# Performance work log

Measured on AMD Instinct MI355X. Metric: run time of the kernel, lower is better.

The kernel has to match this reference:

```python
import jax, jax.numpy as jnp
import numpy as np
import math

# dims
H = 2048        # hidden_size
NH = 16         # mamba_num_heads
HPH = 128       # hidden_size_per_head
I = NH * HPH    # intermediate_size = 2048
N = 64          # mamba_d_state
K = 4           # mamba_d_conv
R = max(64, H // 16)  # time_step_rank = 128
L = 2048        # total tokens (single prefill sequence)
EPS = 1e-6


def rmsnorm(x, w, eps=EPS):
    return x * jax.lax.rsqrt(jnp.mean(x * x, axis=-1, keepdims=True) + eps) * w


def setup_inputs() -> dict:
    key = jax.random.key(0)
    ks = jax.random.split(key, 12)
    s = 0.02
    # dt_bias per get_initial_dt_bias
    dt_min, dt_max = 0.001, 0.1
    u = jax.random.uniform(ks[0], (NH,))
    dt = jnp.exp(u * (math.log(dt_max) - math.log(dt_min)) + math.log(dt_min))
    dt = jnp.clip(dt, 0.0001)
    dt_bias = dt + jnp.log(-jnp.expm1(-dt))
    return {
        "hidden_states": jax.random.normal(ks[1], (L, H), jnp.float32),
        "in_proj_w": jax.random.normal(ks[2], (H, 2 * I), jnp.float32) * s,
        "conv_w": jax.random.normal(ks[3], (I, K), jnp.float32) * s,
        "bcdt_w": jax.random.normal(ks[4], (I, 2 * N + R), jnp.float32) * s,
        "dt_norm_w": jnp.ones((R,), jnp.float32),
        "B_norm_w": jnp.ones((N,), jnp.float32),
        "C_norm_w": jnp.ones((N,), jnp.float32),
        "dt_proj_w": jax.random.normal(ks[5], (R, NH), jnp.float32) * s,
        "dt_bias": dt_bias.astype(jnp.float32),
        "A": -jnp.exp(jax.random.normal(ks[6], (I, N), jnp.float32) * 0.5),  # A = -exp(A_log)
        "D": jnp.ones((I,), jnp.float32),
        "out_proj_w": jax.random.normal(ks[7], (I, H), jnp.float32) * s,
    }


def reference(hidden_states, in_proj_w, conv_w, bcdt_w, dt_norm_w, B_norm_w,
              C_norm_w, dt_proj_w, dt_bias, A, D, out_proj_w):
    # in_proj -> [L, NH, 2*HPH]; split into gate and hidden (per-head halves)
    proj = (hidden_states @ in_proj_w).reshape(L, NH, 2 * HPH)
    gate = proj[:, :, :HPH].reshape(L, I)
    hs = proj[:, :, HPH:].reshape(L, I)

    # causal depthwise conv1d along time + SiLU
    xp = jnp.pad(hs, ((K - 1, 0), (0, 0)))  # left-pad time (zero initial conv state)
    conv = sum(conv_w[:, k] * xp[k:k + L] for k in range(K))  # [L, I]
    hs = jax.nn.silu(conv)

    # B, C, dt projections + RMSNorms
    ssm_p = hs @ bcdt_w  # [L, 2N+R]
    B = rmsnorm(ssm_p[:, :N], B_norm_w)          # [L, N]
    C = rmsnorm(ssm_p[:, N:2 * N], C_norm_w)     # [L, N]
    ts = rmsnorm(ssm_p[:, 2 * N:], dt_norm_w)    # [L, R]
    dt = ts @ dt_proj_w                           # [L, NH]

    # expand per-head dt / bias to full intermediate dim, softplus discretization
    dt_full = jnp.repeat(dt, HPH, axis=1)         # [L, I]
    bias_full = jnp.repeat(dt_bias, HPH)          # [I]
    delta = jax.nn.softplus(dt_full + bias_full)  # [L, I]

    # selective scan: state [I, N], zero initial state
    def step(state, xs):
        u_t, d_t, B_t, C_t = xs
        dA = jnp.exp(d_t[:, None] * A)                      # [I, N]
        state = state * dA + (d_t * u_t)[:, None] * B_t[None, :]
        y_t = state @ C_t                                    # [I]
        return state, y_t

    state0 = jnp.zeros((I, N), jnp.float32)
    _, ys = jax.lax.scan(step, state0, (hs, delta, B, C))    # ys: [L, I]

    y = ys + D * hs
    y = y * jax.nn.silu(gate)
    return y @ out_proj_w  # [L, H]
```

## Files before the change

### kernel.cpp

```cpp
#include <hip/hip_runtime.h>
#include <hip/hip_bf16.h>

#define L_   2048
#define H_   2048
#define I_   2048
#define NH_  16
#define HPH_ 128
#define NS_  64
#define R_   128
#define NCH_ 64
#define CT_  32

typedef __attribute__((ext_vector_type(8))) short s16x8;
typedef __attribute__((ext_vector_type(4))) float f32x4;

__device__ __forceinline__ short f2bf(float x) {
  unsigned u = __builtin_bit_cast(unsigned, x);
  u += 0x7fff + ((u >> 16) & 1);
  return (short)(u >> 16);
}

__device__ __forceinline__ void gll16(const void* g, void* l) {
  __builtin_amdgcn_global_load_lds(
      (__attribute__((address_space(1))) void*)(void*)g,
      (__attribute__((address_space(3))) void*)l, 16, 0, 0);
}

__global__ __launch_bounds__(256) void pack_w(const float* __restrict__ W,
                                              short* __restrict__ Wp,
                                              int KN, int logN) {
  int idx = blockIdx.x * 256 + threadIdx.x;
  if (idx >= KN) return;
  int k = idx >> logN;
  int n = idx & ((1 << logN) - 1);
  Wp[((size_t)(k >> 3) << (logN + 3)) + ((size_t)n << 3) + (k & 7)] = f2bf(W[idx]);
}

__global__ __launch_bounds__(256) void cast_bf(const float* __restrict__ X,
                                               short* __restrict__ Xb, int nElem) {
  int idx = blockIdx.x * 256 + threadIdx.x;
  if (idx < nElem) Xb[idx] = f2bf(X[idx]);
}

template<int BM>
__global__ __launch_bounds__(256) void gemm_st(const short* __restrict__ A,
                                               const short* __restrict__ Bp,
                                               float* __restrict__ C,
                                               int M, int N, int K) {
  constexpr int MI = BM / 32;
  __shared__ short sA[BM * 64];
  __shared__ short sB[8 * 128 * 8];
  int tid = threadIdx.x;
  int lane = tid & 63, wid = tid >> 6;
  int wr = wid >> 1, wc = wid & 1;
  int l15 = lane & 15, l16 = lane >> 4;
  int bm = blockIdx.x * BM, bn = blockIdx.y * 128;

  f32x4 acc[MI][4] = {};

  int arow = lane >> 3;
  int acolb = ((lane & 7) ^ arow) * 16;
  const char* Ag = (const char*)(A + (size_t)bm * K) + acolb;
  const char* Bg = (const char*)(Bp + (size_t)bn * 8);

  for (int k0 = 0; k0 < K; k0 += 64) {
    __syncthreads();
#pragma unroll
    for (int q = 0; q < BM / 32; ++q) {
      int rbase = (q * 4 + wid) * 8;
      gll16(Ag + ((size_t)(rbase + arow) * K + k0) * 2,
            (char*)sA + rbase * 128);
    }
#pragma unroll
    for (int q = 0; q < 4; ++q) {
      int c = q * 4 + wid;
      int kg = c >> 1, nh = (c & 1) * 64;
      gll16(Bg + ((size_t)(k0 / 8 + kg) * N * 8 + (size_t)(nh + lane) * 8) * 2,
            (char*)sB + kg * 2048 + nh * 16);
    }
    __syncthreads();

#pragma unroll
    for (int kk = 0; kk < 64; kk += 32) {
      s16x8 a[MI], b[4];
#pragma unroll
      for (int mi = 0; mi < MI; ++mi) {
        int row = wr * (BM / 2) + mi * 16 + l15;
        int kb = ((kk + l16 * 8) * 2) ^ ((row & 7) << 4);
        a[mi] = *(const s16x8*)((const char*)sA + row * 128 + kb);
      }
#pragma unroll
      for (int ni = 0; ni < 4; ++ni) {
        int n = wc * 64 + ni * 16 + l15;
        int kg = (kk >> 3) + l16;
        b[ni] = *(const s16x8*)((const char*)sB + (kg * 128 + n) * 16);
      }
#pragma unroll
      for (int mi = 0; mi < MI; ++mi)
#pragma unroll
        for (int ni = 0; ni < 4; ++ni)
          acc[mi][ni] = __builtin_amdgcn_mfma_f32_16x16x32_bf16(a[mi], b[ni], acc[mi][ni], 0, 0, 0);
    }
  }
#pragma unroll
  for (int mi = 0; mi < MI; ++mi) {
    int row0 = bm + wr * (BM / 2) + mi * 16 + l16 * 4;
#pragma unroll
    for (int ni = 0; ni < 4; ++ni) {
      int col = bn + wc * 64 + ni * 16 + l15;
#pragma unroll
      for (int r = 0; r < 4; ++r)
        C[(size_t)(row0 + r) * N + col] = acc[mi][ni][r];
    }
  }
}

__global__ __launch_bounds__(256) void conv_silu(const float* __restrict__ proj,
                                                 const float* __restrict__ convw,
                                                 float* __restrict__ hs,
                                                 short* __restrict__ hsb,
                                                 float* __restrict__ gate_s) {
  int idx = blockIdx.x * 256 + threadIdx.x;
  int t = idx >> 11, i = idx & (I_ - 1);
  int col = ((i >> 7) << 8) + 128 + (i & 127);
  float4 cw = *(const float4*)(convw + i * 4);
  const float* p = proj + (size_t)t * (2 * I_) + col;
  float acc = cw.w * p[0];
  if (t >= 1) acc += cw.z * p[-(2 * I_)];
  if (t >= 2) acc += cw.y * p[-(2 * I_) * 2];
  if (t >= 3) acc += cw.x * p[-(2 * I_) * 3];
  float h = acc / (1.f + __expf(-acc));
  hs[idx] = h;
  hsb[idx] = f2bf(h);
  float g = p[-128];
  gate_s[idx] = g / (1.f + __expf(-g));
}

__global__ __launch_bounds__(256) void norm_dt(const float* __restrict__ sp,
                                               const float* __restrict__ Bw,
                                               const float* __restrict__ Cw,
                                               const float* __restrict__ dtw,
                                               const float* __restrict__ Wdt,
                                               const float* __restrict__ bias,
                                               float* __restrict__ Bo,
                                               float* __restrict__ Co,
                                               float* __restrict__ delta) {
  int lane = threadIdx.x & 63, w = threadIdx.x >> 6;
  int t = blockIdx.x * 4 + w;
  const float* row = sp + (size_t)t * 256;
  float v0 = row[lane], v1 = row[64 + lane], v2 = row[128 + lane], v3 = row[192 + lane];
  float sB = v0 * v0, sC = v1 * v1, sT = v2 * v2 + v3 * v3;
#pragma unroll
  for (int off = 32; off; off >>= 1) {
    sB += __shfl_xor(sB, off);
    sC += __shfl_xor(sC, off);
    sT += __shfl_xor(sT, off);
  }
  float rB = rsqrtf(sB * (1.f / 64) + 1e-6f);
  float rC = rsqrtf(sC * (1.f / 64) + 1e-6f);
  float rT = rsqrtf(sT * (1.f / 128) + 1e-6f);
  Bo[t * 64 + lane] = v0 * rB * Bw[lane];
  Co[t * 64 + lane] = v1 * rC * Cw[lane];
  float t2 = v2 * rT * dtw[lane], t3 = v3 * rT * dtw[64 + lane];
  float p[NH_];
  const float* w0 = Wdt + lane * NH_;
  const float* w1 = Wdt + (64 + lane) * NH_;
#pragma unroll
  for (int h = 0; h < NH_; ++h) p[h] = t2 * w0[h] + t3 * w1[h];
#pragma unroll
  for (int off = 32; off; off >>= 1)
#pragma unroll
    for (int h = 0; h < NH_; ++h) p[h] += __shfl_xor(p[h], off);
  if (lane == 0) {
#pragma unroll
    for (int h = 0; h < NH_; ++h) {
      float x = p[h] + bias[h];
      delta[t * NH_ + h] = (x > 20.f) ? x : log1pf(__expf(x));
    }
  }
}

__global__ __launch_bounds__(512) void chunk_sums(const float* __restrict__ delta,
                                                  float* __restrict__ sumd) {
  int t = blockIdx.x * 512 + threadIdx.x;
  int c = t >> 4, h = t & 15;
  float s = 0.f;
  const float* p = delta + (size_t)c * CT_ * NH_ + h;
#pragma unroll 8
  for (int j = 0; j < CT_; ++j) s += p[(size_t)j * NH_];
  sumd[t] = s;
}

__device__ __forceinline__ float rdlane(float v, int l) {
  return __builtin_bit_cast(float, __builtin_amdgcn_readlane(__builtin_bit_cast(int, v), l));
}

__global__ __launch_bounds__(256) void scan1(const float* __restrict__ hs,
                                             const float* __restrict__ Bm,
                                             const float* __restrict__ delta,
                                             const float* __restrict__ A,
                                             float* __restrict__ st) {
  __shared__ float sB[CT_ * 64];
  int tid = threadIdx.x;
  int lane = tid & 63, wv = tid >> 6;
  int c0 = blockIdx.x * 256 + wv * 64;
  int cl = lane & 31, nh = lane >> 5;
  int chunk = blockIdx.y;
  int t0 = chunk * CT_;
  int head = c0 >> 7;
  int i0 = c0 + cl, i1 = i0 + 32;
  int nb = nh * 32;

  { const float4* B4 = (const float4*)(Bm + (size_t)t0 * 64);
    float4* S4 = (float4*)sB;
    S4[tid] = B4[tid];
    S4[256 + tid] = B4[256 + tid]; }
  float d_r = delta[(size_t)(t0 + cl) * NH_ + head];

  float a0[32], a1[32], s0[32], s1[32];
#pragma unroll
  for (int q = 0; q < 8; ++q) {
    float4 av = *(const float4*)&A[(size_t)i0 * 64 + nb + q * 4];
    float4 aw = *(const float4*)&A[(size_t)i1 * 64 + nb + q * 4];
    a0[q*4+0]=av.x; a0[q*4+1]=av.y; a0[q*4+2]=av.z; a0[q*4+3]=av.w;
    a1[q*4+0]=aw.x; a1[q*4+1]=aw.y; a1[q*4+2]=aw.z; a1[q*4+3]=aw.w;
  }
#pragma unroll
  for (int n = 0; n < 32; ++n) { s0[n] = 0.f; s1[n] = 0.f; }
  __syncthreads();

  const float* up = hs + (size_t)t0 * I_;
  float u0n = up[i0], u1n = up[i1];
#pragma unroll 1
  for (int t = 0; t < CT_; ++t) {
    float u0 = u0n, u1 = u1n;
    u0n = up[(size_t)(t + 1) * I_ + i0];
    u1n = up[(size_t)(t + 1) * I_ + i1];
    float dlt = rdlane(d_r, t);
    float du0 = dlt * u0, du1 = dlt * u1;
    const float* bt = &sB[t * 64 + nb];
#pragma unroll
    for (int q = 0; q < 8; ++q) {
      float4 b4 = *(const float4*)&bt[q * 4];
#pragma unroll
      for (int j = 0; j < 4; ++j) {
        int n = q * 4 + j; float bb = (&b4.x)[j];
        s0[n] = s0[n] * __expf(dlt * a0[n]) + du0 * bb;
        s1[n] = s1[n] * __expf(dlt * a1[n]) + du1 * bb;
      }
    }
  }
  size_t base = ((size_t)chunk << 17) + i0;
#pragma unroll
  for (int n = 0; n < 32; ++n) {
    st[base + ((size_t)(nb + n) << 11)] = s0[n];
    st[base + ((size_t)(nb + n) << 11) + 32] = s1[n];
  }
}

__global__ __launch_bounds__(512) void scan2(const float* __restrict__ A,
                                             const float* __restrict__ sumd,
                                             float* __restrict__ st) {
  int g = blockIdx.x * 512 + threadIdx.x;
  int i = g & (I_ - 1), n = g >> 11;
  int h = i >> 7;
  float aV = A[((size_t)i << 6) + n];
  float s = 0.f;
#pragma unroll 1
  for (int c = 0; c < NCH_; ++c) {
    float gfac = __expf(aV * sumd[c * 16 + h]);
    float loc = st[((size_t)c << 17) + g];
    st[((size_t)c << 17) + g] = s;
    s = s * gfac + loc;
  }
}

__global__ __launch_bounds__(256) void scan3(const float* __restrict__ hs,
                                             const float* __restrict__ Bm,
                                             const float* __restrict__ Cm,
                                             const float* __restrict__ delta,
                                             const float* __restrict__ A,
                                             const float* __restrict__ Dv,
                                             const float* __restrict__ gate_s,
                                             const float* __restrict__ st,
                                             short* __restrict__ ybf) {
  __shared__ float sB[CT_ * 64], sC[CT_ * 64];
  int tid = threadIdx.x;
  int lane = tid & 63, wv = tid >> 6;
  int c0 = blockIdx.x * 256 + wv * 64;
  int cl = lane & 31, nh = lane >> 5;
  int chunk = blockIdx.y;
  int t0 = chunk * CT_;
  int head = c0 >> 7;
  int i0 = c0 + cl, i1 = i0 + 32;
  int nb = nh * 32;

  { const float4* B4 = (const float4*)(Bm + (size_t)t0 * 64);
    const float4* C4 = (const float4*)(Cm + (size_t)t0 * 64);
    float4* SB4 = (float4*)sB;
    float4* SC4 = (float4*)sC;
    SB4[tid] = B4[tid];       SB4[256 + tid] = B4[256 + tid];
    SC4[tid] = C4[tid];       SC4[256 + tid] = C4[256 + tid]; }
  float d_r = delta[(size_t)(t0 + cl) * NH_ + head];
  float D_own = Dv[c0 + lane];

  float a0[32], a1[32], s0[32], s1[32];
#pragma unroll
  for (int q = 0; q < 8; ++q) {
    float4 av = *(const float4*)&A[(size_t)i0 * 64 + nb + q * 4];
    float4 aw = *(const float4*)&A[(size_t)i1 * 64 + nb + q * 4];
    a0[q*4+0]=av.x; a0[q*4+1]=av.y; a0[q*4+2]=av.z; a0[q*4+3]=av.w;
    a1[q*4+0]=aw.x; a1[q*4+1]=aw.y; a1[q*4+2]=aw.z; a1[q*4+3]=aw.w;
  }
  { size_t base = ((size_t)chunk << 17) + i0;
#pragma unroll
    for (int n = 0; n < 32; ++n) {
      s0[n] = st[base + ((size_t)(nb + n) << 11)];
      s1[n] = st[base + ((size_t)(nb + n) << 11) + 32];
    } }
  __syncthreads();

  const float* up = hs + (size_t)t0 * I_;
  const float* gp = gate_s + (size_t)t0 * I_ + c0 + lane;
  short* yp = ybf + (size_t)t0 * I_ + c0 + lane;
  float u0n = up[i0], u1n = up[i1];
#pragma unroll 1
  for (int t = 0; t < CT_; ++t) {
    float u0 = u0n, u1 = u1n;
    u0n = up[(size_t)(t + 1) * I_ + i0];
    u1n = up[(size_t)(t + 1) * I_ + i1];
    float gv = gp[(size_t)t * I_];
    float dlt = rdlane(d_r, t);
    float du0 = dlt * u0, du1 = dlt * u1;
    const float* bt = &sB[t * 64 + nb];
    const float* ct = &sC[t * 64 + nb];
    float p0 = 0.f, p1 = 0.f;
#pragma unroll
    for (int q = 0; q < 8; ++q) {
      float4 b4 = *(const float4*)&bt[q * 4];
      float4 c4 = *(const float4*)&ct[q * 4];
#pragma unroll
      for (int j = 0; j < 4; ++j) {
        int n = q * 4 + j;
        float bb = (&b4.x)[j], cc = (&c4.x)[j];
        s0[n] = s0[n] * __expf(dlt * a0[n]) + du0 * bb;
        p0 += s0[n] * cc;
        s1[n] = s1[n] * __expf(dlt * a1[n]) + du1 * bb;
        p1 += s1[n] * cc;
      }
    }
    float snd = (lane < 32) ? p1 : p0;
    snd = __shfl_xor(snd, 32);
    float y = ((lane < 32) ? p0 : p1) + snd;
    float u_own = (lane < 32) ? u0 : u1;
    y += D_own * u_own;
    yp[(size_t)t * I_] = f2bf(y * gv);
  }
}

extern "C" void kernel_launch(void* const* d_in, const int* in_sizes, int n_in,
                              void* d_out, int out_size, void* d_ws, size_t ws_size,
                              hipStream_t stream) {
  const float* hidden  = (const float*)d_in[0];
  const float* inproj  = (const float*)d_in[1];
  const float* convw   = (const float*)d_in[2];
  const float* bcdtw   = (const float*)d_in[3];
  const float* dtnw    = (const float*)d_in[4];
  const float* Bnw     = (const float*)d_in[5];
  const float* Cnw     = (const float*)d_in[6];
  const float* dtpw    = (const float*)d_in[7];
  const float* dtbias  = (const float*)d_in[8];
  const float* Amat    = (const float*)d_in[9];
  const float* Dvec    = (const float*)d_in[10];
  const float* outproj = (const float*)d_in[11];
  float* out = (float*)d_out;

  char* ws = (char*)d_ws;
  short* inproj_p  = (short*)ws; ws += (size_t)H_ * 2 * I_ * 2;
  short* bcdt_p    = (short*)ws; ws += (size_t)I_ * 256 * 2;
  short* outproj_p = (short*)ws; ws += (size_t)I_ * H_ * 2;
  short* hid_b     = (short*)ws; ws += (size_t)L_ * H_ * 2;
  float* proj      = (float*)ws; ws += (size_t)L_ * 2 * I_ * 4;
  float* hs        = (float*)ws; ws += (size_t)(L_ + 1) * I_ * 4;
  short* hs_b      = (short*)ws; ws += (size_t)L_ * I_ * 2;
  float* gate_s    = (float*)ws; ws += (size_t)L_ * I_ * 4;
  float* ssmp      = (float*)ws; ws += (size_t)L_ * 256 * 4;
  float* Bmat      = (float*)ws; ws += (size_t)L_ * NS_ * 4;
  float* Cmat      = (float*)ws; ws += (size_t)L_ * NS_ * 4;
  float* delta     = (float*)ws; ws += (size_t)L_ * NH_ * 4;
  short* y_b       = (short*)ws; ws += (size_t)L_ * I_ * 2;
  float* sumd      = (float*)ws; ws += NCH_ * 16 * 4;
  float* sstate    = (float*)proj;

  pack_w<<<(H_ * 2 * I_ + 255) / 256, 256, 0, stream>>>(inproj, inproj_p, H_ * 2 * I_, 12);
  pack_w<<<(I_ * 256 + 255) / 256, 256, 0, stream>>>(bcdtw, bcdt_p, I_ * 256, 8);
  pack_w<<<(I_ * H_ + 255) / 256, 256, 0, stream>>>(outproj, outproj_p, I_ * H_, 11);
  cast_bf<<<(L_ * H_ + 255) / 256, 256, 0, stream>>>(hidden, hid_b, L_ * H_);

  gemm_st<128><<<dim3(L_ / 128, (2 * I_) / 128), 256, 0, stream>>>(hid_b, inproj_p, proj, L_, 2 * I_, H_);
  conv_silu<<<(L_ * I_) / 256, 256, 0, stream>>>(proj, convw, hs, hs_b, gate_s);
  gemm_st<64><<<dim3(L_ / 64, 256 / 128), 256, 0, stream>>>(hs_b, bcdt_p, ssmp, L_, 256, I_);
  norm_dt<<<L_ / 4, 256, 0, stream>>>(ssmp, Bnw, Cnw, dtnw, dtpw, dtbias, Bmat, Cmat, delta);

  chunk_sums<<<(NCH_ * 16) / 512, 512, 0, stream>>>(delta, sumd);
  scan1<<<dim3(I_ / 256, NCH_), 256, 0, stream>>>(hs, Bmat, delta, Amat, sstate);
  scan2<<<(I_ * 64) / 512, 512, 0, stream>>>(Amat, sumd, sstate);
  scan3<<<dim3(I_ / 256, NCH_), 256, 0, stream>>>(hs, Bmat, Cmat, delta, Amat, Dvec, gate_s, sstate, y_b);

  gemm_st<64><<<dim3(L_ / 64, H_ / 128), 256, 0, stream>>>(y_b, outproj_p, out, L_, H_, I_);
}
```

Baseline: 310.4 us.

## Remap scan lanes to 4 channels x 16 states, prescale A by log2e, batch scan2 loads

The chunked scan kernels now give each lane 4 channels × 16 states instead of 2 channels × 32 states. The per-timestep output is reduced with two xor-shuffles instead of one. A is premultiplied by log2(e) so the decay uses exp2f, which drops a multiply from each exponential. scan2 moves to 256-thread blocks, loads all 64 chunk states into registers up front, and fully unrolls the combine loop to expose memory parallelism. The cost is higher register pressure in scan2 and an extra shuffle stage in scan3.

New measurement: 356.7 us. +14.9%, slower.

```diff
diff --git a/kernel.cpp b/kernel.cpp
--- a/kernel.cpp
+++ b/kernel.cpp
@@ -10,6 +10,7 @@
 #define R_   128
 #define NCH_ 64
 #define CT_  32
+#define LOG2E 1.4426950408889634f
 
 typedef __attribute__((ext_vector_type(8))) short s16x8;
 typedef __attribute__((ext_vector_type(4))) float f32x4;
@@ -191,6 +192,7 @@
   sumd[t] = s;
 }
 
+
 __device__ __forceinline__ float rdlane(float v, int l) {
   return __builtin_bit_cast(float, __builtin_amdgcn_readlane(__builtin_bit_cast(int, v), l));
 }
@@ -203,75 +205,83 @@
   __shared__ float sB[CT_ * 64];
   int tid = threadIdx.x;
   int lane = tid & 63, wv = tid >> 6;
-  int c0 = blockIdx.x * 256 + wv * 64;
-  int cl = lane & 31, nh = lane >> 5;
+  int c0w = blockIdx.x * 256 + wv * 64;
+  int c = lane & 15, q = lane >> 4;
   int chunk = blockIdx.y;
   int t0 = chunk * CT_;
-  int head = c0 >> 7;
-  int i0 = c0 + cl, i1 = i0 + 32;
-  int nb = nh * 32;
+  int head = c0w >> 7;
+  int nb = q * 16;
+  int ch0 = c0w + c;
 
   { const float4* B4 = (const float4*)(Bm + (size_t)t0 * 64);
     float4* S4 = (float4*)sB;
     S4[tid] = B4[tid];
     S4[256 + tid] = B4[256 + tid]; }
-  float d_r = delta[(size_t)(t0 + cl) * NH_ + head];
-
-  float a0[32], a1[32], s0[32], s1[32];
-#pragma unroll
-  for (int q = 0; q < 8; ++q) {
-    float4 av = *(const float4*)&A[(size_t)i0 * 64 + nb + q * 4];
-    float4 aw = *(const float4*)&A[(size_t)i1 * 64 + nb + q * 4];
-    a0[q*4+0]=av.x; a0[q*4+1]=av.y; a0[q*4+2]=av.z; a0[q*4+3]=av.w;
-    a1[q*4+0]=aw.x; a1[q*4+1]=aw.y; a1[q*4+2]=aw.z; a1[q*4+3]=aw.w;
-  }
-#pragma unroll
-  for (int n = 0; n < 32; ++n) { s0[n] = 0.f; s1[n] = 0.f; }
+  float d_r = delta[(size_t)(t0 + (lane & 31)) * NH_ + head];
+
+  float aL[4][16], s[4][16];
+#pragma unroll
+  for (int j = 0; j < 4; ++j) {
+    const float* Ap = A + (size_t)(ch0 + 16 * j) * 64 + nb;
+#pragma unroll
+    for (int k4 = 0; k4 < 4; ++k4) {
+      float4 av = *(const float4*)(Ap + k4 * 4);
+      aL[j][k4*4+0] = av.x * LOG2E; aL[j][k4*4+1] = av.y * LOG2E;
+      aL[j][k4*4+2] = av.z * LOG2E; aL[j][k4*4+3] = av.w * LOG2E;
+    }
+#pragma unroll
+    for (int k = 0; k < 16; ++k) s[j][k] = 0.f;
+  }
   __syncthreads();
 
   const float* up = hs + (size_t)t0 * I_;
-  float u0n = up[i0], u1n = up[i1];
+  float n0 = up[ch0], n1 = up[ch0 + 16], n2 = up[ch0 + 32], n3 = up[ch0 + 48];
 #pragma unroll 1
   for (int t = 0; t < CT_; ++t) {
-    float u0 = u0n, u1 = u1n;
-    u0n = up[(size_t)(t + 1) * I_ + i0];
-    u1n = up[(size_t)(t + 1) * I_ + i1];
+    float u0 = n0, u1 = n1, u2 = n2, u3 = n3;
+    const float* upn = up + (size_t)(t + 1) * I_;
+    n0 = upn[ch0]; n1 = upn[ch0 + 16]; n2 = upn[ch0 + 32]; n3 = upn[ch0 + 48];
     float dlt = rdlane(d_r, t);
-    float du0 = dlt * u0, du1 = dlt * u1;
+    float du0 = dlt * u0, du1 = dlt * u1, du2 = dlt * u2, du3 = dlt * u3;
     const float* bt = &sB[t * 64 + nb];
 #pragma unroll
-    for (int q = 0; q < 8; ++q) {
-      float4 b4 = *(const float4*)&bt[q * 4];
-#pragma unroll
-      for (int j = 0; j < 4; ++j) {
-        int n = q * 4 + j; float bb = (&b4.x)[j];
-        s0[n] = s0[n] * __expf(dlt * a0[n]) + du0 * bb;
-        s1[n] = s1[n] * __expf(dlt * a1[n]) + du1 * bb;
+    for (int k4 = 0; k4 < 4; ++k4) {
+      float4 b4 = *(const float4*)&bt[k4 * 4];
+#pragma unroll
+      for (int e = 0; e < 4; ++e) {
+        int k = k4 * 4 + e; float bb = (&b4.x)[e];
+        s[0][k] = s[0][k] * exp2f(dlt * aL[0][k]) + du0 * bb;
+        s[1][k] = s[1][k] * exp2f(dlt * aL[1][k]) + du1 * bb;
+        s[2][k] = s[2][k] * exp2f(dlt * aL[2][k]) + du2 * bb;
+        s[3][k] = s[3][k] * exp2f(dlt * aL[3][k]) + du3 * bb;
       }
     }
   }
-  size_t base = ((size_t)chunk << 17) + i0;
-#pragma unroll
-  for (int n = 0; n < 32; ++n) {
-    st[base + ((size_t)(nb + n) << 11)] = s0[n];
-    st[base + ((size_t)(nb + n) << 11) + 32] = s1[n];
-  }
-}
-
-__global__ __launch_bounds__(512) void scan2(const float* __restrict__ A,
+  size_t base = ((size_t)chunk << 17) + ch0;
+#pragma unroll
+  for (int j = 0; j < 4; ++j)
+#pragma unroll
+    for (int k = 0; k < 16; ++k)
+      st[base + ((size_t)(nb + k) << 11) + 16 * j] = s[j][k];
+}
+
+__global__ __launch_bounds__(256) void scan2(const float* __restrict__ A,
                                              const float* __restrict__ sumd,
                                              float* __restrict__ st) {
-  int g = blockIdx.x * 512 + threadIdx.x;
+  int g = blockIdx.x * 256 + threadIdx.x;
   int i = g & (I_ - 1), n = g >> 11;
   int h = i >> 7;
-  float aV = A[((size_t)i << 6) + n];
+  float aL = A[((size_t)i << 6) + n] * LOG2E;
+  float loc[NCH_];
+#pragma unroll
+  for (int c = 0; c < NCH_; ++c) loc[c] = st[((size_t)c << 17) + g];
   float s = 0.f;
-#pragma unroll 1
+#pragma unroll
   for (int c = 0; c < NCH_; ++c) {
-    float gfac = __expf(aV * sumd[c * 16 + h]);
-    float loc = st[((size_t)c << 17) + g];
+    float gfac = exp2f(aL * sumd[c * 16 + h]);
+    float nxt = s * gfac + loc[c];
     st[((size_t)c << 17) + g] = s;
-    s = s * gfac + loc;
+    s = nxt;
   }
 }
 
@@ -287,13 +297,13 @@
   __shared__ float sB[CT_ * 64], sC[CT_ * 64];
   int tid = threadIdx.x;
   int lane = tid & 63, wv = tid >> 6;
-  int c0 = blockIdx.x * 256 + wv * 64;
-  int cl = lane & 31, nh = lane >> 5;
+  int c0w = blockIdx.x * 256 + wv * 64;
+  int c = lane & 15, q = lane >> 4;
   int chunk = blockIdx.y;
   int t0 = chunk * CT_;
-  int head = c0 >> 7;
-  int i0 = c0 + cl, i1 = i0 + 32;
-  int nb = nh * 32;
+  int head = c0w >> 7;
+  int nb = q * 16;
+  int ch0 = c0w + c;
 
   { const float4* B4 = (const float4*)(Bm + (size_t)t0 * 64);
     const float4* C4 = (const float4*)(Cm + (size_t)t0 * 64);
@@ -301,58 +311,66 @@
     float4* SC4 = (float4*)sC;
     SB4[tid] = B4[tid];       SB4[256 + tid] = B4[256 + tid];
     SC4[tid] = C4[tid];       SC4[256 + tid] = C4[256 + tid]; }
-  float d_r = delta[(size_t)(t0 + cl) * NH_ + head];
-  float D_own = Dv[c0 + lane];
-
-  float a0[32], a1[32], s0[32], s1[32];
-#pragma unroll
-  for (int q = 0; q < 8; ++q) {
-    float4 av = *(const float4*)&A[(size_t)i0 * 64 + nb + q * 4];
-    float4 aw = *(const float4*)&A[(size_t)i1 * 64 + nb + q * 4];
-    a0[q*4+0]=av.x; a0[q*4+1]=av.y; a0[q*4+2]=av.z; a0[q*4+3]=av.w;
-    a1[q*4+0]=aw.x; a1[q*4+1]=aw.y; a1[q*4+2]=aw.z; a1[q*4+3]=aw.w;
-  }
-  { size_t base = ((size_t)chunk << 17) + i0;
-#pragma unroll
-    for (int n = 0; n < 32; ++n) {
-      s0[n] = st[base + ((size_t)(nb + n) << 11)];
-      s1[n] = st[base + ((size_t)(nb + n) << 11) + 32];
-    } }
+  float d_r = delta[(size_t)(t0 + (lane & 31)) * NH_ + head];
+  float D_own = Dv[c0w + lane];
+
+  float aL[4][16], s[4][16];
+#pragma unroll
+  for (int j = 0; j < 4; ++j) {
+    const float* Ap = A + (size_t)(ch0 + 16 * j) * 64 + nb;
+#pragma unroll
+    for (int k4 = 0; k4 < 4; ++k4) {
+      float4 av = *(const float4*)(Ap + k4 * 4);
+      aL[j][k4*4+0] = av.x * LOG2E; aL[j][k4*4+1] = av.y * LOG2E;
+      aL[j][k4*4+2] = av.z * LOG2E; aL[j][k4*4+3] = av.w * LOG2E;
+    }
+  }
+  { size_t base = ((size_t)chunk << 17) + ch0;
+#pragma unroll
+    for (int j = 0; j < 4; ++j)
+#pragma unroll
+      for (int k = 0; k < 16; ++k)
+        s[j][k] = st[base + ((size_t)(nb + k) << 11) + 16 * j];
+  }
   __syncthreads();
 
   const float* up = hs + (size_t)t0 * I_;
-  const float* gp = gate_s + (size_t)t0 * I_ + c0 + lane;
-  short* yp = ybf + (size_t)t0 * I_ + c0 + lane;
-  float u0n = up[i0], u1n = up[i1];
+  const float* gp = gate_s + (size_t)t0 * I_ + c0w + lane;
+  short* yp = ybf + (size_t)t0 * I_ + c0w + lane;
+  float n0 = up[ch0], n1 = up[ch0 + 16], n2 = up[ch0 + 32], n3 = up[ch0 + 48];
+  bool b4f = lane & 16, b5f = lane & 32;
 #pragma unroll 1
   for (int t = 0; t < CT_; ++t) {
-    float u0 = u0n, u1 = u1n;
-    u0n = up[(size_t)(t + 1) * I_ + i0];
-    u1n = up[(size_t)(t + 1) * I_ + i1];
+    float u0 = n0, u1 = n1, u2 = n2, u3 = n3;
+    const float* upn = up + (size_t)(t + 1) * I_;
+    n0 = upn[ch0]; n1 = upn[ch0 + 16]; n2 = upn[ch0 + 32]; n3 = upn[ch0 + 48];
     float gv = gp[(size_t)t * I_];
     float dlt = rdlane(d_r, t);
-    float du0 = dlt * u0, du1 = dlt * u1;
+    float du0 = dlt * u0, du1 = dlt * u1, du2 = dlt * u2, du3 = dlt * u3;
     const float* bt = &sB[t * 64 + nb];
     const float* ct = &sC[t * 64 + nb];
-    float p0 = 0.f, p1 = 0.f;
-#pragma unroll
-    for (int q = 0; q < 8; ++q) {
-      float4 b4 = *(const float4*)&bt[q * 4];
-      float4 c4 = *(const float4*)&ct[q * 4];
-#pragma unroll
-      for (int j = 0; j < 4; ++j) {
-        int n = q * 4 + j;
-        float bb = (&b4.x)[j], cc = (&c4.x)[j];
-        s0[n] = s0[n] * __expf(dlt * a0[n]) + du0 * bb;
-        p0 += s0[n] * cc;
-        s1[n] = s1[n] * __expf(dlt * a1[n]) + du1 * bb;
-        p1 += s1[n] * cc;
+    float p0 = 0.f, p1 = 0.f, p2 = 0.f, p3 = 0.f;
+#pragma unroll
+    for (int k4 = 0; k4 < 4; ++k4) {
+      float4 b4 = *(const float4*)&bt[k4 * 4];
+      float4 c4 = *(const float4*)&ct[k4 * 4];
+#pragma unroll
+      for (int e = 0; e < 4; ++e) {
+        int k = k4 * 4 + e;
+        float bb = (&b4.x)[e], cc = (&c4.x)[e];
+        s[0][k] = s[0][k] * exp2f(dlt * aL[0][k]) + du0 * bb;  p0 += s[0][k] * cc;
+        s[1][k] = s[1][k] * exp2f(dlt * aL[1][k]) + du1 * bb;  p1 += s[1][k] * cc;
+        s[2][k] = s[2][k] * exp2f(dlt * aL[2][k]) + du2 * bb;  p2 += s[2][k] * cc;
+        s[3][k] = s[3][k] * exp2f(dlt * aL[3][k]) + du3 * bb;  p3 += s[3][k] * cc;
       }
     }
-    float snd = (lane < 32) ? p1 : p0;
-    snd = __shfl_xor(snd, 32);
-    float y = ((lane < 32) ? p0 : p1) + snd;
-    float u_own = (lane < 32) ? u0 : u1;
+    float sa = b5f ? p0 : p2;
+    float sb = b5f ? p1 : p3;
+    float qa = (b5f ? p2 : p0) + __shfl_xor(sa, 32);
+    float qb = (b5f ? p3 : p1) + __shfl_xor(sb, 32);
+    float sc = b4f ? qa : qb;
+    float y  = (b4f ? qb : qa) + __shfl_xor(sc, 16);
+    float u_own = b5f ? (b4f ? u3 : u2) : (b4f ? u1 : u0);
     y += D_own * u_own;
     yp[(size_t)t * I_] = f2bf(y * gv);
   }
@@ -404,7 +422,7 @@
 
   chunk_sums<<<(NCH_ * 16) / 512, 512, 0, stream>>>(delta, sumd);
   scan1<<<dim3(I_ / 256, NCH_), 256, 0, stream>>>(hs, Bmat, delta, Amat, sstate);
-  scan2<<<(I_ * 64) / 512, 512, 0, stream>>>(Amat, sumd, sstate);
+  scan2<<<(I_ * 64) / 256, 256, 0, stream>>>(Amat, sumd, sstate);
   scan3<<<dim3(I_ / 256, NCH_), 256, 0, stream>>>(hs, Bmat, Cmat, delta, Amat, Dvec, gate_s, sstate, y_b);
 
   gemm_st<64><<<dim3(L_ / 64, H_ / 128), 256, 0, stream>>>(y_b, outproj_p, out, L_, H_, I_);
```
